# Kernel optimization log

Measured on AMD Instinct MI355X. Metric: run time of the kernel, lower is better.

## Reference

```python
import jax, jax.numpy as jnp
import numpy as np

B, T, U, QS, MS = 64, 2048, 512, 512, 512

def setup_inputs() -> dict:
    key = jax.random.key(0)
    k1, k2, k3, k4, k5 = jax.random.split(key, 5)
    query = jax.random.normal(k1, (B, QS), dtype=jnp.float32)
    keys = jax.random.normal(k2, (B, T, MS), dtype=jnp.float32)
    # torch nn.Linear weights: [out, in], no bias
    Wq = jax.random.normal(k3, (U, QS), dtype=jnp.float32) * (1.0 / np.sqrt(QS))
    Wm = jax.random.normal(k4, (U, MS), dtype=jnp.float32) * (1.0 / np.sqrt(MS))
    Wa = jax.random.normal(k5, (1, U), dtype=jnp.float32) * (1.0 / np.sqrt(U))
    return {"query": query, "keys": keys, "Wq": Wq, "Wm": Wm, "Wa": Wa}

def reference(query, keys, Wq, Wm, Wa):
    # processed_query: [B, U]
    pq = jnp.einsum('bq,uq->bu', query, Wq)
    # values: [B, T, U]
    vals = jnp.einsum('btm,um->btu', keys, Wm)
    # alignment score: [B, T]
    score = jnp.einsum('btu,u->bt', jnp.tanh(pq[:, None, :] + vals), Wa[0])
    weight = jax.nn.softmax(score, axis=-1)            # [B, T]
    total_context = jnp.einsum('bt,btm->bm', weight, keys)  # [B, MS]
    return (total_context, score)
```

## Files before the change

### kernel.cpp

```cpp
#include <hip/hip_runtime.h>
#include <cstdint>
#include <cstddef>

#define Bn 64
#define Tn 2048
#define Un 512
#define QSn 512
#define MSn 512
#define TCH 64
#define NCH 32
#define NKT 16

using f32x16 = __attribute__((ext_vector_type(16))) float;
using bf16x8 = __attribute__((ext_vector_type(8))) short;

__device__ __forceinline__ unsigned short f2bf(float x) {
    unsigned int u = __float_as_uint(x);
    u += 0x7FFFu + ((u >> 16) & 1u);
    return (unsigned short)(u >> 16);
}

__device__ __forceinline__ unsigned int pk2bf(float lo, float hi) {
    unsigned int r;
    asm("v_cvt_pk_bf16_f32 %0, %1, %2" : "=v"(r) : "v"(lo), "v"(hi));
    return r;
}

__device__ __forceinline__ float tanh_fast(float x) {
    float e = exp2f(x * 2.885390043258667f);
    return 1.f - 2.f * __builtin_amdgcn_rcpf(e + 1.f);
}

#define GLOAD(G, L) __builtin_amdgcn_global_load_lds( \
    (const __attribute__((address_space(1))) void*)(G), \
    (__attribute__((address_space(3))) void*)(L), 16, 0, 0)

#define SB() __builtin_amdgcn_sched_barrier(0)

__global__ __launch_bounds__(256) void cvt_kernel(const float* __restrict__ src,
                                                  unsigned short* __restrict__ dst) {
    int i = blockIdx.x * 256 + threadIdx.x;
    float4 v = *(const float4*)(src + (size_t)i * 4);
    ushort4 h = { f2bf(v.x), f2bf(v.y), f2bf(v.z), f2bf(v.w) };
    *(ushort4*)&dst[(size_t)i * 4] = h;
}

__global__ __launch_bounds__(128) void pq_kernel(const float* __restrict__ query,
                                                 const float* __restrict__ Wq,
                                                 float* __restrict__ pq) {
    __shared__ float ql[QSn];
    const int b = blockIdx.x;
    const int quad = blockIdx.y;
    const int tid = threadIdx.x;
    for (int i = tid; i < QSn; i += 128) ql[i] = query[(size_t)b * QSn + i];
    __syncthreads();
    const int u = quad * 128 + tid;
    const float* w = Wq + (size_t)u * QSn;
    float a0 = 0.f, a1 = 0.f;
    #pragma unroll 4
    for (int k = 0; k < QSn; k += 8) {
        float4 w0 = *(const float4*)(w + k);
        float4 w1 = *(const float4*)(w + k + 4);
        float4 q0 = *(const float4*)(ql + k);
        float4 q1 = *(const float4*)(ql + k + 4);
        a0 += w0.x * q0.x + w0.y * q0.y + w0.z * q0.z + w0.w * q0.w;
        a1 += w1.x * q1.x + w1.y * q1.y + w1.z * q1.z + w1.w * q1.w;
    }
    pq[(size_t)b * Un + u] = a0 + a1;
}

__global__ __launch_bounds__(512, 4) void fused_kernel(const float* __restrict__ keys,
                                                       const unsigned short* __restrict__ WmB,
                                                       const float* __restrict__ pq,
                                                       const float* __restrict__ Wa,
                                                       float* __restrict__ score_out,
                                                       float* __restrict__ pm,
                                                       float* __restrict__ pl,
                                                       float* __restrict__ pctx) {
    __shared__ __align__(16) unsigned short Ah[2][TCH * 32];
    __shared__ __align__(16) unsigned short Bh[2][512 * 32];
    __shared__ float sc_lds[8][TCH];
    __shared__ float stot[TCH];
    __shared__ float wexp[TCH];

    const int tid = threadIdx.x;
    const int lane = tid & 63;
    const int w = tid >> 6;
    const int lc = lane & 31;
    const int l5 = lane >> 5;
    const int b = blockIdx.y;
    const int chunk = blockIdx.x;
    const int t0 = chunk * TCH;

    const int ar = tid >> 3;
    const int kq = tid & 7;
    const int awof = (ar >> 1) * 64 +
                     (((((kq >> 1) << 1) | (ar & 1)) ^ ((ar >> 1) & 7)) * 8) +
                     (kq & 1) * 4;
    const float* gA = keys + ((size_t)b * Tn + t0 + ar) * MSn + kq * 4;

    const int bg = (lane & 7) ^ ((lane >> 3) & 7);
    const unsigned short* gBw = WmB +
        (size_t)(w * 64 + (((lane >> 3) << 1) | (bg & 1))) * MSn + (bg >> 1) * 8;

    #define STAGE_B(KT, BUF) do { \
        const unsigned short* gb_ = gBw + (KT) * 32; \
        char* bD_ = (char*)&Bh[BUF][0] + w * 4096; \
        GLOAD(gb_,                    bD_); \
        GLOAD(gb_ + (size_t)16 * MSn, bD_ + 1024); \
        GLOAD(gb_ + (size_t)32 * MSn, bD_ + 2048); \
        GLOAD(gb_ + (size_t)48 * MSn, bD_ + 3072); } while (0)

    f32x16 acc[2][2];
    #pragma unroll
    for (int mf = 0; mf < 2; ++mf)
        #pragma unroll
        for (int nf = 0; nf < 2; ++nf)
            #pragma unroll
            for (int r = 0; r < 16; ++r) acc[mf][nf][r] = 0.f;

    float pqv[2], wav[2];
    #pragma unroll
    for (int nf = 0; nf < 2; ++nf) {
        int u = w * 64 + nf * 32 + lc;
        pqv[nf] = pq[(size_t)b * Un + u];
        wav[nf] = Wa[u];
    }
    SB();
    {
        float4 p = *(const float4*)(gA);
        SB();
        STAGE_B(0, 0);
        SB();
        uint2 h;
        h.x = pk2bf(p.x, p.y);
        h.y = pk2bf(p.z, p.w);
        *(uint2*)&Ah[0][awof] = h;
    }

    #pragma unroll
    for (int kt = 0; kt < NKT; ++kt) {
        float4 p;
        if (kt < NKT - 1) {
            p = *(const float4*)(gA + (kt + 1) * 32);
            SB();
            STAGE_B(kt + 1, (kt + 1) & 1);
            SB();
            asm volatile("s_waitcnt vmcnt(5) lgkmcnt(0)" ::: "memory");
        } else {
            asm volatile("s_waitcnt vmcnt(0) lgkmcnt(0)" ::: "memory");
        }
        __builtin_amdgcn_s_barrier();
        SB();

        {
            const unsigned short* lA = &Ah[kt & 1][0];
            const unsigned short* lB = &Bh[kt & 1][0];
            #pragma unroll
            for (int ks = 0; ks < 2; ++ks) {
                bf16x8 af[2], bfr[2];
                #pragma unroll
                for (int mf = 0; mf < 2; ++mf) {
                    int r = mf * 32 + lc;
                    int gp = (((ks * 2 + l5) << 1) | (r & 1)) ^ ((r >> 1) & 7);
                    af[mf] = *(const bf16x8*)&lA[(r >> 1) * 64 + gp * 8];
                }
                #pragma unroll
                for (int nf = 0; nf < 2; ++nf) {
                    int ru = w * 64 + nf * 32 + lc;
                    int gp = (((ks * 2 + l5) << 1) | (ru & 1)) ^ ((ru >> 1) & 7);
                    bfr[nf] = *(const bf16x8*)&lB[(ru >> 1) * 64 + gp * 8];
                }
                #pragma unroll
                for (int mf = 0; mf < 2; ++mf)
                    #pragma unroll
                    for (int nf = 0; nf < 2; ++nf)
                        acc[mf][nf] = __builtin_amdgcn_mfma_f32_32x32x16_bf16(
                            af[mf], bfr[nf], acc[mf][nf], 0, 0, 0);
            }
        }
        SB();

        if (kt < NKT - 1) {
            uint2 h;
            h.x = pk2bf(p.x, p.y);
            h.y = pk2bf(p.z, p.w);
            *(uint2*)&Ah[(kt + 1) & 1][awof] = h;
        }
    }
    #undef STAGE_B

    #pragma unroll
    for (int mf = 0; mf < 2; ++mf) {
        #pragma unroll
        for (int r = 0; r < 16; ++r) {
            float s = tanh_fast(acc[mf][0][r] + pqv[0]) * wav[0]
                    + tanh_fast(acc[mf][1][r] + pqv[1]) * wav[1];
            s += __shfl_xor(s, 16);
            s += __shfl_xor(s, 8);
            s += __shfl_xor(s, 4);
            s += __shfl_xor(s, 2);
            s += __shfl_xor(s, 1);
            if (lc == 0)
                sc_lds[w][mf * 32 + (r & 3) + 8 * (r >> 2) + 4 * l5] = s;
        }
    }
    __syncthreads();
    if (tid < TCH) {
        float v = ((sc_lds[0][tid] + sc_lds[1][tid]) + (sc_lds[2][tid] + sc_lds[3][tid]))
                + ((sc_lds[4][tid] + sc_lds[5][tid]) + (sc_lds[6][tid] + sc_lds[7][tid]));
        stot[tid] = v;
        score_out[(size_t)b * Tn + t0 + tid] = v;
    }
    __syncthreads();

    if (tid < 64) {
        float v = stot[tid];
        float mx = v;
        #pragma unroll
        for (int off = 32; off; off >>= 1) mx = fmaxf(mx, __shfl_xor(mx, off));
        float e = __expf(v - mx);
        wexp[tid] = e;
        float sum = e;
        #pragma unroll
        for (int off = 32; off; off >>= 1) sum += __shfl_xor(sum, off);
        if (tid == 0) {
            pm[b * NCH + chunk] = mx;
            pl[b * NCH + chunk] = sum;
        }
    }
    __syncthreads();

    const float* kp = keys + ((size_t)b * Tn + t0) * MSn + tid;
    float cx = 0.f;
    #pragma unroll 8
    for (int t = 0; t < TCH; ++t)
        cx += wexp[t] * kp[(size_t)t * MSn];
    pctx[((size_t)(b * NCH + chunk)) * MSn + tid] = cx;
}

__global__ __launch_bounds__(512) void merge_kernel(const float* __restrict__ pm,
                                                    const float* __restrict__ pl,
                                                    const float* __restrict__ pctx,
                                                    float* __restrict__ ctx) {
    __shared__ float sm[NCH], sl[NCH];
    const int b = blockIdx.x, tid = threadIdx.x;
    if (tid < NCH) {
        sm[tid] = pm[b * NCH + tid];
        sl[tid] = pl[b * NCH + tid];
    }
    __syncthreads();
    float M = -1e30f;
    #pragma unroll
    for (int c = 0; c < NCH; ++c) M = fmaxf(M, sm[c]);
    float L = 0.f;
    #pragma unroll
    for (int c = 0; c < NCH; ++c) L += sl[c] * __expf(sm[c] - M);
    const float inv = 1.f / L;
    float acc = 0.f;
    #pragma unroll
    for (int c = 0; c < NCH; ++c)
        acc += __expf(sm[c] - M) * pctx[((size_t)(b * NCH + c)) * MSn + tid];
    ctx[(size_t)b * MSn + tid] = acc * inv;
}

extern "C" void kernel_launch(void* const* d_in, const int* in_sizes, int n_in,
                              void* d_out, int out_size, void* d_ws, size_t ws_size,
                              hipStream_t stream) {
    const float* query = (const float*)d_in[0];
    const float* keys  = (const float*)d_in[1];
    const float* Wq    = (const float*)d_in[2];
    const float* Wm    = (const float*)d_in[3];
    const float* Wa    = (const float*)d_in[4];

    float* ctx_out   = (float*)d_out;
    float* score_out = (float*)d_out + (size_t)Bn * MSn;

    char* ws = (char*)d_ws;
    float* ws_pq   = (float*)(ws);
    unsigned short* ws_wmbf = (unsigned short*)(ws + 131072);
    float* ws_pm   = (float*)(ws + 655360);
    float* ws_pl   = (float*)(ws + 663552);
    float* ws_pctx = (float*)(ws + 671744);

    cvt_kernel<<<(Un * MSn / 4) / 256, 256, 0, stream>>>(Wm, ws_wmbf);
    pq_kernel<<<dim3(Bn, 4), 128, 0, stream>>>(query, Wq, ws_pq);
    fused_kernel<<<dim3(NCH, Bn), 512, 0, stream>>>(keys, ws_wmbf, ws_pq, Wa,
                                                    score_out, ws_pm, ws_pl, ws_pctx);
    merge_kernel<<<Bn, 512, 0, stream>>>(ws_pm, ws_pl, ws_pctx, ctx_out);
}
```

Before: 167.9 us.

## Halve time chunk and have each wave stage its own fp32 keys via direct LDS loads

Halves the time chunk per block, doubling the grid, and gives each wave its own private LDS slices for keys and Wm. Keys now go straight into LDS as fp32 through global_load_lds and are converted to bf16 when fragments are read, replacing the register round-trip and cross-wave packing. The per-iteration block barrier is dropped because each wave only reads what it staged. In exchange, keys are staged redundantly by all 8 waves, there is no double buffering (a full vmcnt(0) wait each step), and the merge kernel has twice as many partials to combine.

Result: slower. 302.6 us (+80.3%).

```diff
diff --git a/kernel.cpp b/kernel.cpp
--- a/kernel.cpp
+++ b/kernel.cpp
@@ -7,8 +7,8 @@
 #define Un 512
 #define QSn 512
 #define MSn 512
-#define TCH 64
-#define NCH 32
+#define TCH 32
+#define NCH 64
 #define NKT 16
 
 using f32x16 = __attribute__((ext_vector_type(16))) float;
@@ -24,6 +24,15 @@
     unsigned int r;
     asm("v_cvt_pk_bf16_f32 %0, %1, %2" : "=v"(r) : "v"(lo), "v"(hi));
     return r;
+}
+
+__device__ __forceinline__ bf16x8 cvt8(float4 a, float4 b) {
+    union { unsigned int u[4]; bf16x8 v; } r;
+    r.u[0] = pk2bf(a.x, a.y);
+    r.u[1] = pk2bf(a.z, a.w);
+    r.u[2] = pk2bf(b.x, b.y);
+    r.u[3] = pk2bf(b.z, b.w);
+    return r.v;
 }
 
 __device__ __forceinline__ float tanh_fast(float x) {
@@ -77,8 +86,8 @@
                                                        float* __restrict__ pm,
                                                        float* __restrict__ pl,
                                                        float* __restrict__ pctx) {
-    __shared__ __align__(16) unsigned short Ah[2][TCH * 32];
-    __shared__ __align__(16) unsigned short Bh[2][512 * 32];
+    __shared__ __align__(16) float Ah[8][TCH * 32];
+    __shared__ __align__(16) unsigned short Bh[8][64 * 32];
     __shared__ float sc_lds[8][TCH];
     __shared__ float stot[TCH];
     __shared__ float wexp[TCH];
@@ -92,32 +101,40 @@
     const int chunk = blockIdx.x;
     const int t0 = chunk * TCH;
 
-    const int ar = tid >> 3;
-    const int kq = tid & 7;
-    const int awof = (ar >> 1) * 64 +
-                     (((((kq >> 1) << 1) | (ar & 1)) ^ ((ar >> 1) & 7)) * 8) +
-                     (kq & 1) * 4;
-    const float* gA = keys + ((size_t)b * Tn + t0 + ar) * MSn + kq * 4;
+    const float* keyBase = keys + (size_t)(b * Tn + t0) * MSn;
+
+    int aoff[4];
+    #pragma unroll
+    for (int j = 0; j < 4; ++j) {
+        int rp = j * 4 + (lane >> 4);
+        int g = (lane & 15) ^ (rp & 7);
+        aoff[j] = (rp * 2 + (g & 1)) * MSn + (g >> 1) * 4;
+    }
 
     const int bg = (lane & 7) ^ ((lane >> 3) & 7);
     const unsigned short* gBw = WmB +
         (size_t)(w * 64 + (((lane >> 3) << 1) | (bg & 1))) * MSn + (bg >> 1) * 8;
 
-    #define STAGE_B(KT, BUF) do { \
+    #define STAGE_A(KT) do { \
+        char* aD_ = (char*)&Ah[w][0]; \
+        GLOAD(keyBase + (KT) * 32 + aoff[0], aD_); \
+        GLOAD(keyBase + (KT) * 32 + aoff[1], aD_ + 1024); \
+        GLOAD(keyBase + (KT) * 32 + aoff[2], aD_ + 2048); \
+        GLOAD(keyBase + (KT) * 32 + aoff[3], aD_ + 3072); } while (0)
+
+    #define STAGE_B(KT) do { \
         const unsigned short* gb_ = gBw + (KT) * 32; \
-        char* bD_ = (char*)&Bh[BUF][0] + w * 4096; \
+        char* bD_ = (char*)&Bh[w][0]; \
         GLOAD(gb_,                    bD_); \
         GLOAD(gb_ + (size_t)16 * MSn, bD_ + 1024); \
         GLOAD(gb_ + (size_t)32 * MSn, bD_ + 2048); \
         GLOAD(gb_ + (size_t)48 * MSn, bD_ + 3072); } while (0)
 
-    f32x16 acc[2][2];
-    #pragma unroll
-    for (int mf = 0; mf < 2; ++mf)
-        #pragma unroll
-        for (int nf = 0; nf < 2; ++nf)
-            #pragma unroll
-            for (int r = 0; r < 16; ++r) acc[mf][nf][r] = 0.f;
+    f32x16 acc[2];
+    #pragma unroll
+    for (int nf = 0; nf < 2; ++nf)
+        #pragma unroll
+        for (int r = 0; r < 16; ++r) acc[nf][r] = 0.f;
 
     float pqv[2], wav[2];
     #pragma unroll
@@ -127,85 +144,67 @@
         wav[nf] = Wa[u];
     }
     SB();
-    {
-        float4 p = *(const float4*)(gA);
+    STAGE_A(0);
+    STAGE_B(0);
+    SB();
+
+    #pragma unroll
+    for (int kt = 0; kt < NKT; ++kt) {
+        asm volatile("s_waitcnt vmcnt(0)" ::: "memory");
         SB();
-        STAGE_B(0, 0);
-        SB();
-        uint2 h;
-        h.x = pk2bf(p.x, p.y);
-        h.y = pk2bf(p.z, p.w);
-        *(uint2*)&Ah[0][awof] = h;
-    }
-
-    #pragma unroll
-    for (int kt = 0; kt < NKT; ++kt) {
-        float4 p;
-        if (kt < NKT - 1) {
-            p = *(const float4*)(gA + (kt + 1) * 32);
-            SB();
-            STAGE_B(kt + 1, (kt + 1) & 1);
-            SB();
-            asm volatile("s_waitcnt vmcnt(5) lgkmcnt(0)" ::: "memory");
-        } else {
-            asm volatile("s_waitcnt vmcnt(0) lgkmcnt(0)" ::: "memory");
-        }
-        __builtin_amdgcn_s_barrier();
-        SB();
-
+
+        bf16x8 af[2], bfr[2][2];
         {
-            const unsigned short* lA = &Ah[kt & 1][0];
-            const unsigned short* lB = &Bh[kt & 1][0];
+            const float* lA = &Ah[w][0];
+            const unsigned short* lB = &Bh[w][0];
             #pragma unroll
             for (int ks = 0; ks < 2; ++ks) {
-                bf16x8 af[2], bfr[2];
-                #pragma unroll
-                for (int mf = 0; mf < 2; ++mf) {
-                    int r = mf * 32 + lc;
-                    int gp = (((ks * 2 + l5) << 1) | (r & 1)) ^ ((r >> 1) & 7);
-                    af[mf] = *(const bf16x8*)&lA[(r >> 1) * 64 + gp * 8];
-                }
+                int rp = lc >> 1;
+                int kg0 = (ks * 2 + l5) * 2;
+                int g0 = (kg0 << 1) | (lc & 1);
+                int g1 = ((kg0 + 1) << 1) | (lc & 1);
+                float4 f0 = *(const float4*)&lA[rp * 64 + (g0 ^ (rp & 7)) * 4];
+                float4 f1 = *(const float4*)&lA[rp * 64 + (g1 ^ (rp & 7)) * 4];
+                af[ks] = cvt8(f0, f1);
                 #pragma unroll
                 for (int nf = 0; nf < 2; ++nf) {
-                    int ru = w * 64 + nf * 32 + lc;
-                    int gp = (((ks * 2 + l5) << 1) | (ru & 1)) ^ ((ru >> 1) & 7);
-                    bfr[nf] = *(const bf16x8*)&lB[(ru >> 1) * 64 + gp * 8];
+                    int lr = nf * 32 + lc;
+                    int gp = (((ks * 2 + l5) << 1) | (lr & 1)) ^ ((lr >> 1) & 7);
+                    bfr[ks][nf] = *(const bf16x8*)&lB[(lr >> 1) * 64 + gp * 8];
                 }
-                #pragma unroll
-                for (int mf = 0; mf < 2; ++mf)
-                    #pragma unroll
-                    for (int nf = 0; nf < 2; ++nf)
-                        acc[mf][nf] = __builtin_amdgcn_mfma_f32_32x32x16_bf16(
-                            af[mf], bfr[nf], acc[mf][nf], 0, 0, 0);
             }
         }
+        asm volatile("s_waitcnt lgkmcnt(0)" ::: "memory");
         SB();
-
         if (kt < NKT - 1) {
-            uint2 h;
-            h.x = pk2bf(p.x, p.y);
-            h.y = pk2bf(p.z, p.w);
-            *(uint2*)&Ah[(kt + 1) & 1][awof] = h;
-        }
-    }
+            STAGE_A(kt + 1);
+            STAGE_B(kt + 1);
+            SB();
+        }
+
+        #pragma unroll
+        for (int ks = 0; ks < 2; ++ks) {
+            acc[0] = __builtin_amdgcn_mfma_f32_32x32x16_bf16(af[ks], bfr[ks][0], acc[0], 0, 0, 0);
+            acc[1] = __builtin_amdgcn_mfma_f32_32x32x16_bf16(af[ks], bfr[ks][1], acc[1], 0, 0, 0);
+        }
+    }
+    #undef STAGE_A
     #undef STAGE_B
 
     #pragma unroll
-    for (int mf = 0; mf < 2; ++mf) {
-        #pragma unroll
-        for (int r = 0; r < 16; ++r) {
-            float s = tanh_fast(acc[mf][0][r] + pqv[0]) * wav[0]
-                    + tanh_fast(acc[mf][1][r] + pqv[1]) * wav[1];
-            s += __shfl_xor(s, 16);
-            s += __shfl_xor(s, 8);
-            s += __shfl_xor(s, 4);
-            s += __shfl_xor(s, 2);
-            s += __shfl_xor(s, 1);
-            if (lc == 0)
-                sc_lds[w][mf * 32 + (r & 3) + 8 * (r >> 2) + 4 * l5] = s;
-        }
-    }
-    __syncthreads();
+    for (int r = 0; r < 16; ++r) {
+        float s = tanh_fast(acc[0][r] + pqv[0]) * wav[0]
+                + tanh_fast(acc[1][r] + pqv[1]) * wav[1];
+        s += __shfl_xor(s, 16);
+        s += __shfl_xor(s, 8);
+        s += __shfl_xor(s, 4);
+        s += __shfl_xor(s, 2);
+        s += __shfl_xor(s, 1);
+        if (lc == 0)
+            sc_lds[w][(r & 3) + 8 * (r >> 2) + 4 * l5] = s;
+    }
+    __syncthreads();
+
     if (tid < TCH) {
         float v = ((sc_lds[0][tid] + sc_lds[1][tid]) + (sc_lds[2][tid] + sc_lds[3][tid]))
                 + ((sc_lds[4][tid] + sc_lds[5][tid]) + (sc_lds[6][tid] + sc_lds[7][tid]));
@@ -214,16 +213,16 @@
     }
     __syncthreads();
 
-    if (tid < 64) {
+    if (tid < TCH) {
         float v = stot[tid];
         float mx = v;
         #pragma unroll
-        for (int off = 32; off; off >>= 1) mx = fmaxf(mx, __shfl_xor(mx, off));
+        for (int off = 16; off; off >>= 1) mx = fmaxf(mx, __shfl_xor(mx, off));
         float e = __expf(v - mx);
         wexp[tid] = e;
         float sum = e;
         #pragma unroll
-        for (int off = 32; off; off >>= 1) sum += __shfl_xor(sum, off);
+        for (int off = 16; off; off >>= 1) sum += __shfl_xor(sum, off);
         if (tid == 0) {
             pm[b * NCH + chunk] = mx;
             pl[b * NCH + chunk] = sum;
@@ -231,7 +230,7 @@
     }
     __syncthreads();
 
-    const float* kp = keys + ((size_t)b * Tn + t0) * MSn + tid;
+    const float* kp = keyBase + tid;
     float cx = 0.f;
     #pragma unroll 8
     for (int t = 0; t < TCH; ++t)
@@ -280,8 +279,8 @@
     float* ws_pq   = (float*)(ws);
     unsigned short* ws_wmbf = (unsigned short*)(ws + 131072);
     float* ws_pm   = (float*)(ws + 655360);
-    float* ws_pl   = (float*)(ws + 663552);
-    float* ws_pctx = (float*)(ws + 671744);
+    float* ws_pl   = (float*)(ws + 671744);
+    float* ws_pctx = (float*)(ws + 688128);
 
     cvt_kernel<<<(Un * MSn / 4) / 256, 256, 0, stream>>>(Wm, ws_wmbf);
     pq_kernel<<<dim3(Bn, 4), 128, 0, stream>>>(query, Wq, ws_pq);
```

## Pre-convert keys to bf16 and stage A tiles with async global-to-LDS loads

Applied to the files above, without the earlier changes.

Adds a separate kernel that converts the whole fp32 keys tensor to bf16 in workspace. The fused kernel then loads A tiles straight into a triple-buffered LDS ring with global_load_lds, issued by four of the eight waves, instead of doing register loads plus in-kernel conversion. The context reduction also reads the bf16 keys. This removes per-tile conversion and register staging from the GEMM loop, but adds a full extra pass over keys (fp32 read plus bf16 write) and lowers the precision of the context sum.

Result: slower. 219.0 us (+30.5%).

```diff
diff --git a/kernel.cpp b/kernel.cpp
--- a/kernel.cpp
+++ b/kernel.cpp
@@ -26,6 +26,10 @@
     return r;
 }
 
+__device__ __forceinline__ float b2f(unsigned short h) {
+    return __uint_as_float(((unsigned int)h) << 16);
+}
+
 __device__ __forceinline__ float tanh_fast(float x) {
     float e = exp2f(x * 2.885390043258667f);
     return 1.f - 2.f * __builtin_amdgcn_rcpf(e + 1.f);
@@ -43,6 +47,19 @@
     float4 v = *(const float4*)(src + (size_t)i * 4);
     ushort4 h = { f2bf(v.x), f2bf(v.y), f2bf(v.z), f2bf(v.w) };
     *(ushort4*)&dst[(size_t)i * 4] = h;
+}
+
+__global__ __launch_bounds__(256) void cvtkeys_kernel(const float* __restrict__ src,
+                                                      unsigned short* __restrict__ dst) {
+    size_t i = ((size_t)blockIdx.x * 256 + threadIdx.x) * 8;
+    float4 v0 = *(const float4*)(src + i);
+    float4 v1 = *(const float4*)(src + i + 4);
+    union { unsigned int u[4]; bf16x8 v; } h;
+    h.u[0] = pk2bf(v0.x, v0.y);
+    h.u[1] = pk2bf(v0.z, v0.w);
+    h.u[2] = pk2bf(v1.x, v1.y);
+    h.u[3] = pk2bf(v1.z, v1.w);
+    *(bf16x8*)&dst[i] = h.v;
 }
 
 __global__ __launch_bounds__(128) void pq_kernel(const float* __restrict__ query,
@@ -69,7 +86,7 @@
     pq[(size_t)b * Un + u] = a0 + a1;
 }
 
-__global__ __launch_bounds__(512, 4) void fused_kernel(const float* __restrict__ keys,
+__global__ __launch_bounds__(512, 4) void fused_kernel(const unsigned short* __restrict__ keysB,
                                                        const unsigned short* __restrict__ WmB,
                                                        const float* __restrict__ pq,
                                                        const float* __restrict__ Wa,
@@ -77,7 +94,7 @@
                                                        float* __restrict__ pm,
                                                        float* __restrict__ pl,
                                                        float* __restrict__ pctx) {
-    __shared__ __align__(16) unsigned short Ah[2][TCH * 32];
+    __shared__ __align__(16) unsigned short Ah[3][TCH * 32];
     __shared__ __align__(16) unsigned short Bh[2][512 * 32];
     __shared__ float sc_lds[8][TCH];
     __shared__ float stot[TCH];
@@ -92,16 +109,13 @@
     const int chunk = blockIdx.x;
     const int t0 = chunk * TCH;
 
-    const int ar = tid >> 3;
-    const int kq = tid & 7;
-    const int awof = (ar >> 1) * 64 +
-                     (((((kq >> 1) << 1) | (ar & 1)) ^ ((ar >> 1) & 7)) * 8) +
-                     (kq & 1) * 4;
-    const float* gA = keys + ((size_t)b * Tn + t0 + ar) * MSn + kq * 4;
-
     const int bg = (lane & 7) ^ ((lane >> 3) & 7);
-    const unsigned short* gBw = WmB +
-        (size_t)(w * 64 + (((lane >> 3) << 1) | (bg & 1))) * MSn + (bg >> 1) * 8;
+    const int srow2 = ((lane >> 3) << 1) | (bg & 1);
+    const int scol8 = (bg >> 1) * 8;
+
+    const unsigned short* gAw = keysB +
+        (size_t)(b * Tn + t0 + w * 16 + srow2) * MSn + scol8;
+    const unsigned short* gBw = WmB + (size_t)(w * 64 + srow2) * MSn + scol8;
 
     #define STAGE_B(KT, BUF) do { \
         const unsigned short* gb_ = gBw + (KT) * 32; \
@@ -111,6 +125,9 @@
         GLOAD(gb_ + (size_t)32 * MSn, bD_ + 2048); \
         GLOAD(gb_ + (size_t)48 * MSn, bD_ + 3072); } while (0)
 
+    #define STAGE_A(KT, RING) do { \
+        GLOAD(gAw + (KT) * 32, (char*)&Ah[RING][0] + w * 1024); } while (0)
+
     f32x16 acc[2][2];
     #pragma unroll
     for (int mf = 0; mf < 2; ++mf)
@@ -126,27 +143,20 @@
         pqv[nf] = pq[(size_t)b * Un + u];
         wav[nf] = Wa[u];
     }
+    asm volatile("s_waitcnt vmcnt(0)" ::: "memory");
     SB();
-    {
-        float4 p = *(const float4*)(gA);
-        SB();
-        STAGE_B(0, 0);
-        SB();
-        uint2 h;
-        h.x = pk2bf(p.x, p.y);
-        h.y = pk2bf(p.z, p.w);
-        *(uint2*)&Ah[0][awof] = h;
-    }
+    if (w < 4) STAGE_A(0, 0);
+    STAGE_B(0, 0);
+    SB();
 
     #pragma unroll
     for (int kt = 0; kt < NKT; ++kt) {
-        float4 p;
         if (kt < NKT - 1) {
-            p = *(const float4*)(gA + (kt + 1) * 32);
-            SB();
+            if (w < 4) STAGE_A(kt + 1, (kt + 1) % 3);
             STAGE_B(kt + 1, (kt + 1) & 1);
             SB();
-            asm volatile("s_waitcnt vmcnt(5) lgkmcnt(0)" ::: "memory");
+            if (w < 4) asm volatile("s_waitcnt vmcnt(5) lgkmcnt(0)" ::: "memory");
+            else       asm volatile("s_waitcnt vmcnt(4) lgkmcnt(0)" ::: "memory");
         } else {
             asm volatile("s_waitcnt vmcnt(0) lgkmcnt(0)" ::: "memory");
         }
@@ -154,7 +164,7 @@
         SB();
 
         {
-            const unsigned short* lA = &Ah[kt & 1][0];
+            const unsigned short* lA = &Ah[kt % 3][0];
             const unsigned short* lB = &Bh[kt & 1][0];
             #pragma unroll
             for (int ks = 0; ks < 2; ++ks) {
@@ -179,15 +189,8 @@
                             af[mf], bfr[nf], acc[mf][nf], 0, 0, 0);
             }
         }
-        SB();
-
-        if (kt < NKT - 1) {
-            uint2 h;
-            h.x = pk2bf(p.x, p.y);
-            h.y = pk2bf(p.z, p.w);
-            *(uint2*)&Ah[(kt + 1) & 1][awof] = h;
-        }
-    }
+    }
+    #undef STAGE_A
     #undef STAGE_B
 
     #pragma unroll
@@ -231,11 +234,11 @@
     }
     __syncthreads();
 
-    const float* kp = keys + ((size_t)b * Tn + t0) * MSn + tid;
+    const unsigned short* kp = keysB + (size_t)(b * Tn + t0) * MSn + tid;
     float cx = 0.f;
     #pragma unroll 8
     for (int t = 0; t < TCH; ++t)
-        cx += wexp[t] * kp[(size_t)t * MSn];
+        cx += wexp[t] * b2f(kp[(size_t)t * MSn]);
     pctx[((size_t)(b * NCH + chunk)) * MSn + tid] = cx;
 }
 
@@ -282,10 +285,12 @@
     float* ws_pm   = (float*)(ws + 655360);
     float* ws_pl   = (float*)(ws + 663552);
     float* ws_pctx = (float*)(ws + 671744);
+    unsigned short* ws_keysB = (unsigned short*)(ws + 4866048);
 
     cvt_kernel<<<(Un * MSn / 4) / 256, 256, 0, stream>>>(Wm, ws_wmbf);
     pq_kernel<<<dim3(Bn, 4), 128, 0, stream>>>(query, Wq, ws_pq);
-    fused_kernel<<<dim3(NCH, Bn), 512, 0, stream>>>(keys, ws_wmbf, ws_pq, Wa,
+    cvtkeys_kernel<<<(Bn * Tn * MSn / 8) / 256, 256, 0, stream>>>(keys, ws_keysB);
+    fused_kernel<<<dim3(NCH, Bn), 512, 0, stream>>>(ws_keysB, ws_wmbf, ws_pq, Wa,
                                                     score_out, ws_pm, ws_pl, ws_pctx);
     merge_kernel<<<Bn, 512, 0, stream>>>(ws_pm, ws_pl, ws_pctx, ctx_out);
 }
```
